# Optimization experiments

Measured on AMD Instinct MI355X. Metric: run time of the kernel, lower is better.

Reference implementation:

```python
import jax, jax.numpy as jnp
import numpy as np

T, B, A = 128, 512, 5
X, Y, Z, H, R = 2, 10, 32, 128, 128
LOG2PI = np.float32(np.log(2.0 * np.pi))


def setup_inputs() -> dict:
    key = jax.random.key(0)
    ks = iter(jax.random.split(key, 40))
    w = lambda *s: jax.random.normal(next(ks), s, jnp.float32) * 0.05
    return dict(
        states=jax.random.normal(next(ks), (T, B, Y), jnp.float32),
        eps=jax.random.normal(next(ks), (T - 1, B, A, Z), jnp.float32),
        enc_w1=w(A, X + Y + R, H), enc_b1=w(A, H),
        enc_w2=w(A, H, H), enc_b2=w(A, H),
        enc_mw=w(A, H, Z), enc_mb=w(A, Z),
        enc_sw=w(A, H, Z), enc_sb=w(A, Z),
        pri_w1=w(A, Y + R, H), pri_b1=w(A, H),
        pri_w2=w(A, H, H), pri_b2=w(A, H),
        pri_mw=w(A, H, Z), pri_mb=w(A, Z),
        pri_sw=w(A, H, Z), pri_sb=w(A, Z),
        dec_w1=w(A, Y + Z + R, H), dec_b1=w(A, H),
        dec_w2=w(A, H, H), dec_b2=w(A, H),
        dec_mw=w(A, H, X), dec_mb=w(A, X),
        dec_sw=w(A, H, X), dec_sb=w(A, X),
        gru_wih=w(A, X + Z, 3 * R), gru_whh=w(A, R, 3 * R),
        gru_bih=w(A, 3 * R), gru_bhh=w(A, 3 * R),
    )


def _lin(x, wt, b):
    # x: [B, A, I], wt: [A, I, O] -> [B, A, O]  (per-agent linear)
    return jnp.einsum('bai,aio->bao', x, wt) + b


def _mlp(x, w1, b1, w2, b2):
    return jax.nn.relu(_lin(jax.nn.relu(_lin(x, w1, b1)), w2, b2))


def reference(states, eps, enc_w1, enc_b1, enc_w2, enc_b2, enc_mw, enc_mb,
              enc_sw, enc_sb, pri_w1, pri_b1, pri_w2, pri_b2, pri_mw, pri_mb,
              pri_sw, pri_sb, dec_w1, dec_b1, dec_w2, dec_b2, dec_mw, dec_mb,
              dec_sw, dec_sb, gru_wih, gru_whh, gru_bih, gru_bhh):
    y_all = states[:-1]                              # [T-1, B, Y]
    x_all = states[1:].reshape(T - 1, B, A, X)       # per-agent next positions

    def step(carry, xs):
        h, kl, nll = carry                           # h: [B, A, R]
        y, x, e = xs                                 # y:[B,Y] x:[B,A,X] e:[B,A,Z]
        yb = jnp.broadcast_to(y[:, None, :], (B, A, Y))
        enc_h = _mlp(jnp.concatenate([x, yb, h], -1), enc_w1, enc_b1, enc_w2, enc_b2)
        enc_m = _lin(enc_h, enc_mw, enc_mb)
        enc_s = jax.nn.softplus(_lin(enc_h, enc_sw, enc_sb))
        pri_h = _mlp(jnp.concatenate([yb, h], -1), pri_w1, pri_b1, pri_w2, pri_b2)
        pri_m = _lin(pri_h, pri_mw, pri_mb)
        pri_s = jax.nn.softplus(_lin(pri_h, pri_sw, pri_sb))
        z = enc_m + enc_s * e                         # reparameterized sample
        dec_h = _mlp(jnp.concatenate([yb, z, h], -1), dec_w1, dec_b1, dec_w2, dec_b2)
        dec_m = _lin(dec_h, dec_mw, dec_mb)
        dec_s = jax.nn.softplus(_lin(dec_h, dec_sw, dec_sb))
        # GRU cell (torch gate order: r, z, n)
        gi = _lin(jnp.concatenate([x, z], -1), gru_wih, gru_bih)   # [B,A,3R]
        gh = _lin(h, gru_whh, gru_bhh)
        gir, giz, gin = jnp.split(gi, 3, -1)
        ghr, ghz, ghn = jnp.split(gh, 3, -1)
        r = jax.nn.sigmoid(gir + ghr)
        u = jax.nn.sigmoid(giz + ghz)
        n = jnp.tanh(gin + r * ghn)
        h_new = (1.0 - u) * n + u * h
        kl_t = 0.5 * jnp.sum(2.0 * jnp.log(pri_s) - 2.0 * jnp.log(enc_s)
                             + (enc_s ** 2 + (enc_m - pri_m) ** 2) / pri_s ** 2 - 1.0)
        nll_t = jnp.sum(0.5 * LOG2PI + jnp.log(dec_s) + 0.5 * ((x - dec_m) / dec_s) ** 2)
        return (h_new, kl + kl_t, nll + nll_t), None

    h0 = jnp.zeros((B, A, R), states.dtype)
    zero = jnp.zeros((), states.dtype)
    (h, kl, nll), _ = jax.lax.scan(step, (h0, zero, zero), (y_all, x_all, eps))
    return jnp.stack([kl, nll])  # [kl_loss, recon_loss]
```

## Files before the change

### kernel.cpp

```cpp
#include <hip/hip_runtime.h>

typedef __attribute__((ext_vector_type(8))) short bf16x8;
typedef __attribute__((ext_vector_type(4))) float f32x4;

#define MFMA_B16(A,B,C) __builtin_amdgcn_mfma_f32_16x16x32_bf16((A),(B),(C),0,0,0)

#define FO_ENC1 0
#define FO_PRI1 48
#define FO_DEC1 88
#define FO_GIH  136
#define FO_GHH  184
#define FO_ENC2 280
#define FO_PRI2 312
#define FO_DEC2 344
#define FO_MS   376
#define FO_DECMS 408
#define NFRAG   412

#define MS  200
#define TS  136

__device__ __forceinline__ unsigned short f2bf(float f) {
  union { float f; unsigned u; } v; v.f = f;
  unsigned r = (v.u + 0x7fffu + ((v.u >> 16) & 1u)) >> 16;
  return (unsigned short)r;
}
__device__ __forceinline__ float bf2f(unsigned short h) {
  union { unsigned u; float f; } v; v.u = ((unsigned)h) << 16;
  return v.f;
}
__device__ __forceinline__ float sigm_(float x) { return 1.f / (1.f + __expf(-x)); }
__device__ __forceinline__ float tanh_(float x) {
  x = fminf(fmaxf(x, -15.f), 15.f);
  float e = __expf(-2.f * x);
  return (1.f - e) / (1.f + e);
}
__device__ __forceinline__ float splus_(float x) {
  return fmaxf(x, 0.f) + log1pf(__expf(-fabsf(x)));
}
__device__ __forceinline__ void pin(bf16x8 &x) {
  f32x4 &r = reinterpret_cast<f32x4&>(x);
  asm volatile("" : "+v"(r));
}
__device__ __forceinline__ void pinf(float &x) { asm volatile("" : "+v"(x)); }

__global__ void prep_kernel(const float* __restrict__ ew1, const float* __restrict__ pw1,
                            const float* __restrict__ dw1, const float* __restrict__ wih,
                            const float* __restrict__ whh, const float* __restrict__ ew2,
                            const float* __restrict__ pw2, const float* __restrict__ dw2,
                            const float* __restrict__ emw, const float* __restrict__ esw,
                            const float* __restrict__ pmw, const float* __restrict__ psw,
                            const float* __restrict__ dmw, const float* __restrict__ dsw,
                            unsigned short* __restrict__ ws)
{
  int blk = blockIdx.x;
  int a = blk / NFRAG, f = blk % NFRAG;
  int l = threadIdx.x, lg = l >> 4, ln = l & 15;
  float v[8];

  if (f < FO_PRI1) {
    int fi = f, nt = fi / 6, kb = fi % 6, n = nt * 16 + ln;
#pragma unroll
    for (int j = 0; j < 8; ++j) {
      int mk = kb * 32 + lg * 8 + j;
      int r = (mk < 2) ? mk : (mk >= 34 && mk < 44) ? 2 + (mk - 34)
            : (mk >= 64) ? 12 + (mk - 64) : -1;
      v[j] = (r >= 0) ? ew1[((size_t)a * 140 + r) * 128 + n] : 0.f;
    }
  } else if (f < FO_DEC1) {
    int fi = f - FO_PRI1, nt = fi / 5, kb = 1 + fi % 5, n = nt * 16 + ln;
#pragma unroll
    for (int j = 0; j < 8; ++j) {
      int mk = kb * 32 + lg * 8 + j;
      int r = (mk >= 34 && mk < 44) ? (mk - 34) : (mk >= 64) ? 10 + (mk - 64) : -1;
      v[j] = (r >= 0) ? pw1[((size_t)a * 138 + r) * 128 + n] : 0.f;
    }
  } else if (f < FO_GIH) {
    int fi = f - FO_DEC1, nt = fi / 6, kb = fi % 6, n = nt * 16 + ln;
#pragma unroll
    for (int j = 0; j < 8; ++j) {
      int mk = kb * 32 + lg * 8 + j;
      int r = (mk >= 2 && mk < 34) ? 10 + (mk - 2) : (mk >= 34 && mk < 44) ? (mk - 34)
            : (mk >= 64) ? 42 + (mk - 64) : -1;
      v[j] = (r >= 0) ? dw1[((size_t)a * 170 + r) * 128 + n] : 0.f;
    }
  } else if (f < FO_GHH) {
    int fi = f - FO_GIH, nt = fi / 2, kb = fi % 2, n = nt * 16 + ln;
#pragma unroll
    for (int j = 0; j < 8; ++j) {
      int mk = kb * 32 + lg * 8 + j;
      v[j] = (mk < 34) ? wih[((size_t)a * 34 + mk) * 384 + n] : 0.f;
    }
  } else if (f < FO_ENC2) {
    int fi = f - FO_GHH, nt = fi / 4, kb = fi % 4, n = nt * 16 + ln;
#pragma unroll
    for (int j = 0; j < 8; ++j) {
      int r = kb * 32 + lg * 8 + j;
      v[j] = whh[((size_t)a * 128 + r) * 384 + n];
    }
  } else if (f < FO_DEC2) {
    int fi = f - FO_ENC2;
    const float* W = (fi < 32) ? ew2 : pw2;
    fi &= 31;
    int nt = fi / 4, kb = fi % 4, n = nt * 16 + ln;
#pragma unroll
    for (int j = 0; j < 8; ++j) {
      int r = kb * 32 + lg * 8 + j;
      v[j] = W[((size_t)a * 128 + r) * 128 + n];
    }
  } else if (f < FO_MS) {
    int fi = f - FO_DEC2, nt = fi / 4, kb = fi % 4, n = nt * 16 + ln;
#pragma unroll
    for (int j = 0; j < 8; ++j) {
      int r = kb * 32 + lg * 8 + j;
      v[j] = dw2[((size_t)a * 128 + r) * 128 + n];
    }
  } else if (f < FO_DECMS) {
    int fi = f - FO_MS, mat = fi / 8, rem = fi % 8, nt = rem / 4, kb = rem % 4;
    int n = nt * 16 + ln;
    const float* W = (mat == 0) ? emw : (mat == 1) ? esw : (mat == 2) ? pmw : psw;
#pragma unroll
    for (int j = 0; j < 8; ++j) {
      int r = kb * 32 + lg * 8 + j;
      v[j] = W[((size_t)a * 128 + r) * 32 + n];
    }
  } else {
    int kb = f - FO_DECMS;
#pragma unroll
    for (int j = 0; j < 8; ++j) {
      int r = kb * 32 + lg * 8 + j;
      v[j] = (ln < 2) ? dmw[((size_t)a * 128 + r) * 2 + ln]
           : (ln < 4) ? dsw[((size_t)a * 128 + r) * 2 + (ln - 2)] : 0.f;
    }
  }
  unsigned short* dst = ws + (size_t)blk * 512 + l * 8;
#pragma unroll
  for (int j = 0; j < 8; ++j) dst[j] = f2bf(v[j]);
}

__global__
__attribute__((amdgpu_flat_work_group_size(512, 512)))
__attribute__((amdgpu_waves_per_eu(2, 2)))
void vrnn_main(
    const float* __restrict__ states, const float* __restrict__ eps,
    const float* __restrict__ eb1, const float* __restrict__ eb2,
    const float* __restrict__ emb, const float* __restrict__ esb,
    const float* __restrict__ pb1, const float* __restrict__ pb2,
    const float* __restrict__ pmb, const float* __restrict__ psb,
    const float* __restrict__ db1, const float* __restrict__ db2,
    const float* __restrict__ dmb, const float* __restrict__ dsb,
    const float* __restrict__ bih, const float* __restrict__ bhh,
    const unsigned short* __restrict__ frags, float* __restrict__ out)
{
  const int a = blockIdx.y;
  const int b0 = blockIdx.x * 16;
  const int tid = threadIdx.x;
  const int w = tid >> 6, l = tid & 63, lg = l >> 4, ln = l & 15;

  __shared__ __align__(16) unsigned short ghh_lds[96 * 512];
  __shared__ __align__(16) unsigned short ms_lds[32 * 512];
  __shared__ __align__(16) unsigned short dms_lds[4 * 512];
  __shared__ __align__(16) unsigned short master[16 * MS];
  __shared__ __align__(16) unsigned short t1e[16 * TS], t1p[16 * TS];
  __shared__ __align__(16) unsigned short he[16 * TS], hp[16 * TS];
  __shared__ float msbuf[2][16][32];
  __shared__ float red[16];

  const unsigned short* fa = frags + (size_t)a * NFRAG * 512;

  {
    const uint4* s1 = (const uint4*)(fa + (size_t)FO_GHH * 512);
    uint4* d1 = (uint4*)ghh_lds;
    for (int i = tid; i < 96 * 64; i += 512) d1[i] = s1[i];
    const uint4* s2 = (const uint4*)(fa + (size_t)FO_MS * 512);
    uint4* d2 = (uint4*)ms_lds;
    for (int i = tid; i < 32 * 64; i += 512) d2[i] = s2[i];
    const uint4* s3 = (const uint4*)(fa + (size_t)FO_DECMS * 512);
    uint4* d3 = (uint4*)dms_lds;
    if (tid < 256) d3[tid] = s3[tid];
  }
  for (int i = tid; i < 16 * MS; i += 512) master[i] = 0;

  bf16x8 be1[6], bp1[5], be2[4], bp2[4], bd2[4], bD[12];
#pragma unroll
  for (int kb = 0; kb < 6; ++kb) {
    be1[kb] = *(const bf16x8*)(fa + (size_t)(FO_ENC1 + w * 6 + kb) * 512 + l * 8);
    pin(be1[kb]);
  }
#pragma unroll
  for (int kb = 0; kb < 5; ++kb) {
    bp1[kb] = *(const bf16x8*)(fa + (size_t)(FO_PRI1 + w * 5 + kb) * 512 + l * 8);
    pin(bp1[kb]);
  }
#pragma unroll
  for (int kb = 0; kb < 4; ++kb) {
    be2[kb] = *(const bf16x8*)(fa + (size_t)(FO_ENC2 + w * 4 + kb) * 512 + l * 8);
    bp2[kb] = *(const bf16x8*)(fa + (size_t)(FO_PRI2 + w * 4 + kb) * 512 + l * 8);
    bd2[kb] = *(const bf16x8*)(fa + (size_t)(FO_DEC2 + w * 4 + kb) * 512 + l * 8);
    pin(be2[kb]); pin(bp2[kb]); pin(bd2[kb]);
  }
  if (w < 4) {
#pragma unroll
    for (int j = 0; j < 2; ++j)
#pragma unroll
      for (int kb = 0; kb < 6; ++kb)
        bD[j * 6 + kb] = *(const bf16x8*)(fa + (size_t)(FO_DEC1 + (w + 4 * j) * 6 + kb) * 512 + l * 8);
  } else {
    int kx = w - 4;
#pragma unroll
    for (int g = 0; g < 3; ++g)
#pragma unroll
      for (int j = 0; j < 2; ++j)
#pragma unroll
        for (int kb = 0; kb < 2; ++kb)
          bD[g * 4 + j * 2 + kb] =
            *(const bf16x8*)(fa + (size_t)(FO_GIH + (g * 8 + kx + 4 * j) * 2 + kb) * 512 + l * 8);
  }
#pragma unroll
  for (int i = 0; i < 12; ++i) pin(bD[i]);

  float eb1v = eb1[a * 128 + w * 16 + ln], pb1v = pb1[a * 128 + w * 16 + ln];
  float eb2v = eb2[a * 128 + w * 16 + ln], pb2v = pb2[a * 128 + w * 16 + ln];
  float db2v = db2[a * 128 + w * 16 + ln];
  float hbm = 0.f, hbs = 0.f, d1b0 = 0.f, d1b1 = 0.f, dmsb = 0.f;
  float ghb[6] = {0.f, 0.f, 0.f, 0.f, 0.f, 0.f};
  if (w < 2) { hbm = emb[a * 32 + w * 16 + ln]; hbs = esb[a * 32 + w * 16 + ln]; }
  else if (w < 4) { hbm = pmb[a * 32 + (w - 2) * 16 + ln]; hbs = psb[a * 32 + (w - 2) * 16 + ln]; }
  if (w < 4) { d1b0 = db1[a * 128 + w * 16 + ln]; d1b1 = db1[a * 128 + (w + 4) * 16 + ln]; }
  else {
    int kx = w - 4;
#pragma unroll
    for (int g = 0; g < 3; ++g)
#pragma unroll
      for (int j = 0; j < 2; ++j)
        ghb[g * 2 + j] = bih[a * 384 + g * 128 + (kx + 4 * j) * 16 + ln]
                       + bhh[a * 384 + g * 128 + (kx + 4 * j) * 16 + ln];
  }
  if (w == 0) dmsb = (ln < 2) ? dmb[a * 2 + ln] : (ln < 4) ? dsb[a * 2 + (ln - 2)] : 0.f;
  pinf(eb1v); pinf(pb1v); pinf(eb2v); pinf(pb2v); pinf(db2v);
  pinf(hbm); pinf(hbs); pinf(d1b0); pinf(d1b1); pinf(dmsb);
#pragma unroll
  for (int i = 0; i < 6; ++i) pinf(ghb[i]);

  __syncthreads();

  if (tid < 160) {
    int row = tid / 10, c = tid - row * 10;
    master[row * MS + 34 + c] = f2bf(states[(size_t)b0 * 10 + tid]);
  }
  if (tid >= 192 && tid < 224) {
    int i = tid - 192, row = i >> 1, c = i & 1;
    master[row * MS + c] = f2bf(states[((size_t)512 + b0 + row) * 10 + a * 2 + c]);
  }
  float e_cur[4] = {0.f, 0.f, 0.f, 0.f};
  if (w < 2) {
#pragma unroll
    for (int q = 0; q < 4; ++q)
      e_cur[q] = eps[((size_t)(b0 + 4 * lg + q) * 5 + a) * 32 + w * 16 + ln];
  }
  float xv[4] = {0.f, 0.f, 0.f, 0.f};
  float kl = 0.f, nll = 0.f;
  f32x4 em = {0, 0, 0, 0}, esv = {0, 0, 0, 0};
  f32x4 gh[3][2];
  float hn[8];
  __syncthreads();

  for (int t = 0; t < 127; ++t) {
    if (w == 0 && t > 0) {
      f32x4 acc = {dmsb, dmsb, dmsb, dmsb};
#pragma unroll
      for (int kb = 0; kb < 4; ++kb) {
        bf16x8 ad = *(const bf16x8*)&he[ln * TS + kb * 32 + lg * 8];
        bf16x8 bf = *(const bf16x8*)&dms_lds[kb * 512 + l * 8];
        acc = MFMA_B16(ad, bf, acc);
      }
#pragma unroll
      for (int q = 0; q < 4; ++q) {
        float sv = __shfl(splus_(acc[q]), l + 2);
        if (ln < 2) {
          float d = (xv[q] - acc[q]) / sv;
          nll += 0.9189385332f + __logf(sv) + 0.5f * d * d;
        }
      }
    }
    {
      bf16x8 am[6];
#pragma unroll
      for (int kb = 0; kb < 6; ++kb)
        am[kb] = *(const bf16x8*)&master[ln * MS + kb * 32 + lg * 8];
      f32x4 a1 = {eb1v, eb1v, eb1v, eb1v}, a2 = {pb1v, pb1v, pb1v, pb1v};
#pragma unroll
      for (int kb = 0; kb < 6; ++kb) a1 = MFMA_B16(am[kb], be1[kb], a1);
#pragma unroll
      for (int kb = 0; kb < 5; ++kb) a2 = MFMA_B16(am[kb + 1], bp1[kb], a2);
#pragma unroll
      for (int q = 0; q < 4; ++q) {
        t1e[(4 * lg + q) * TS + w * 16 + ln] = f2bf(fmaxf(a1[q], 0.f));
        t1p[(4 * lg + q) * TS + w * 16 + ln] = f2bf(fmaxf(a2[q], 0.f));
      }
    }
    __syncthreads();

    {
      bf16x8 ae[4], ap[4];
#pragma unroll
      for (int kb = 0; kb < 4; ++kb) {
        ae[kb] = *(const bf16x8*)&t1e[ln * TS + kb * 32 + lg * 8];
        ap[kb] = *(const bf16x8*)&t1p[ln * TS + kb * 32 + lg * 8];
      }
      f32x4 a1 = {eb2v, eb2v, eb2v, eb2v}, a2 = {pb2v, pb2v, pb2v, pb2v};
#pragma unroll
      for (int kb = 0; kb < 4; ++kb) {
        a1 = MFMA_B16(ae[kb], be2[kb], a1);
        a2 = MFMA_B16(ap[kb], bp2[kb], a2);
      }
#pragma unroll
      for (int q = 0; q < 4; ++q) {
        he[(4 * lg + q) * TS + w * 16 + ln] = f2bf(fmaxf(a1[q], 0.f));
        hp[(4 * lg + q) * TS + w * 16 + ln] = f2bf(fmaxf(a2[q], 0.f));
      }
    }
    __syncthreads();

    {
      if (w < 4) {
        const unsigned short* hsrc = (w < 2) ? he : hp;
        bf16x8 ah[4];
#pragma unroll
        for (int kb = 0; kb < 4; ++kb)
          ah[kb] = *(const bf16x8*)&hsrc[ln * TS + kb * 32 + lg * 8];
        int mbase = ((w < 2) ? 0 : 16) + (w & 1) * 4;
        f32x4 m = {hbm, hbm, hbm, hbm}, s = {hbs, hbs, hbs, hbs};
#pragma unroll
        for (int kb = 0; kb < 4; ++kb) {
          m = MFMA_B16(ah[kb], *(const bf16x8*)&ms_lds[(mbase + kb) * 512 + l * 8], m);
          s = MFMA_B16(ah[kb], *(const bf16x8*)&ms_lds[(mbase + 8 + kb) * 512 + l * 8], s);
        }
        if (w < 2) {
          em = m;
#pragma unroll
          for (int q = 0; q < 4; ++q) {
            esv[q] = splus_(s[q]);
            master[(4 * lg + q) * MS + 2 + w * 16 + ln] = f2bf(m[q] + esv[q] * e_cur[q]);
          }
          if (t < 126) {
#pragma unroll
            for (int q = 0; q < 4; ++q)
              e_cur[q] = eps[((size_t)((t + 1) * 512 + b0 + 4 * lg + q) * 5 + a) * 32 + w * 16 + ln];
          }
        } else {
#pragma unroll
          for (int q = 0; q < 4; ++q) {
            msbuf[0][4 * lg + q][(w - 2) * 16 + ln] = m[q];
            msbuf[1][4 * lg + q][(w - 2) * 16 + ln] = splus_(s[q]);
          }
        }
      } else {
        int kx = w - 4;
        bf16x8 ahh[4];
#pragma unroll
        for (int kb = 0; kb < 4; ++kb)
          ahh[kb] = *(const bf16x8*)&master[ln * MS + (kb + 2) * 32 + lg * 8];
#pragma unroll
        for (int g = 0; g < 3; ++g)
#pragma unroll
          for (int j = 0; j < 2; ++j) {
            float bv = ghb[g * 2 + j];
            gh[g][j] = (f32x4){bv, bv, bv, bv};
          }
#pragma unroll
        for (int kb = 0; kb < 4; ++kb)
#pragma unroll
          for (int g = 0; g < 3; ++g)
#pragma unroll
            for (int j = 0; j < 2; ++j)
              gh[g][j] = MFMA_B16(ahh[kb],
                *(const bf16x8*)&ghh_lds[(size_t)((g * 8 + kx + 4 * j) * 4 + kb) * 512 + l * 8],
                gh[g][j]);
      }
    }
    __syncthreads();

    if (w == 0) {
#pragma unroll
      for (int q = 0; q < 4; ++q)
        xv[q] = states[((size_t)(t + 1) * 512 + b0 + 4 * lg + q) * 10 + a * 2 + (ln & 1)];
    }
    if (w < 4) {
      bf16x8 amn[6];
#pragma unroll
      for (int kb = 0; kb < 6; ++kb)
        amn[kb] = *(const bf16x8*)&master[ln * MS + kb * 32 + lg * 8];
#pragma unroll
      for (int j = 0; j < 2; ++j) {
        float bv = (j == 0) ? d1b0 : d1b1;
        f32x4 acc = {bv, bv, bv, bv};
#pragma unroll
        for (int kb = 0; kb < 6; ++kb) acc = MFMA_B16(amn[kb], bD[j * 6 + kb], acc);
#pragma unroll
        for (int q = 0; q < 4; ++q)
          t1e[(4 * lg + q) * TS + (w + 4 * j) * 16 + ln] = f2bf(fmaxf(acc[q], 0.f));
      }
      if (w < 2) {
#pragma unroll
        for (int q = 0; q < 4; ++q) {
          float pm = msbuf[0][4 * lg + q][w * 16 + ln];
          float ps = msbuf[1][4 * lg + q][w * 16 + ln];
          float dm = em[q] - pm;
          float es2 = esv[q] * esv[q];
          kl += 0.5f * (2.f * __logf(ps) - 2.f * __logf(esv[q]) + (es2 + dm * dm) / (ps * ps) - 1.f);
        }
      }
    } else {
      int kx = w - 4;
      bf16x8 am2[2];
#pragma unroll
      for (int kb = 0; kb < 2; ++kb)
        am2[kb] = *(const bf16x8*)&master[ln * MS + kb * 32 + lg * 8];
      f32x4 gi[3][2];
#pragma unroll
      for (int g = 0; g < 3; ++g)
#pragma unroll
        for (int j = 0; j < 2; ++j) gi[g][j] = (f32x4){0.f, 0.f, 0.f, 0.f};
#pragma unroll
      for (int kb = 0; kb < 2; ++kb)
#pragma unroll
        for (int g = 0; g < 3; ++g)
#pragma unroll
          for (int j = 0; j < 2; ++j)
            gi[g][j] = MFMA_B16(am2[kb], bD[g * 4 + j * 2 + kb], gi[g][j]);
#pragma unroll
      for (int j = 0; j < 2; ++j)
#pragma unroll
        for (int q = 0; q < 4; ++q) {
          float r_ = sigm_(gi[0][j][q] + gh[0][j][q]);
          float u_ = sigm_(gi[1][j][q] + gh[1][j][q]);
          float n_ = tanh_(gi[2][j][q] + r_ * gh[2][j][q]);
          float ho = bf2f(master[(4 * lg + q) * MS + 64 + (kx + 4 * j) * 16 + ln]);
          hn[j * 4 + q] = (1.f - u_) * n_ + u_ * ho;
        }
    }
    __syncthreads();

    {
      bf16x8 ad[4];
#pragma unroll
      for (int kb = 0; kb < 4; ++kb)
        ad[kb] = *(const bf16x8*)&t1e[ln * TS + kb * 32 + lg * 8];
      f32x4 acc = {db2v, db2v, db2v, db2v};
#pragma unroll
      for (int kb = 0; kb < 4; ++kb) acc = MFMA_B16(ad[kb], bd2[kb], acc);
#pragma unroll
      for (int q = 0; q < 4; ++q)
        he[(4 * lg + q) * TS + w * 16 + ln] = f2bf(fmaxf(acc[q], 0.f));
    }
    if (w >= 4) {
      int kx = w - 4;
#pragma unroll
      for (int j = 0; j < 2; ++j)
#pragma unroll
        for (int q = 0; q < 4; ++q)
          master[(4 * lg + q) * MS + 64 + (kx + 4 * j) * 16 + ln] = f2bf(hn[j * 4 + q]);
    }
    if (t < 126) {
      if (w >= 1 && w <= 3) {
        int i = (w - 1) * 64 + l;
        if (i < 160) {
          int row = i / 10, c = i - row * 10;
          master[row * MS + 34 + c] = f2bf(states[((size_t)(t + 1) * 512 + b0) * 10 + i]);
        }
      }
      if (w == 0 && l < 32) {
        int row = l >> 1, c = l & 1;
        master[row * MS + c] = f2bf(states[((size_t)(t + 2) * 512 + b0 + row) * 10 + a * 2 + c]);
      }
    }
    __syncthreads();
  }

  if (w == 0) {
    f32x4 acc = {dmsb, dmsb, dmsb, dmsb};
#pragma unroll
    for (int kb = 0; kb < 4; ++kb) {
      bf16x8 ad = *(const bf16x8*)&he[ln * TS + kb * 32 + lg * 8];
      bf16x8 bf = *(const bf16x8*)&dms_lds[kb * 512 + l * 8];
      acc = MFMA_B16(ad, bf, acc);
    }
#pragma unroll
    for (int q = 0; q < 4; ++q) {
      float sv = __shfl(splus_(acc[q]), l + 2);
      if (ln < 2) {
        float d = (xv[q] - acc[q]) / sv;
        nll += 0.9189385332f + __logf(sv) + 0.5f * d * d;
      }
    }
  }

#pragma unroll
  for (int off = 32; off > 0; off >>= 1) {
    kl += __shfl_down(kl, off);
    nll += __shfl_down(nll, off);
  }
  if (l == 0) { red[w] = kl; red[8 + w] = nll; }
  __syncthreads();
  if (tid == 0) {
    float K = 0.f, N = 0.f;
#pragma unroll
    for (int i = 0; i < 8; ++i) { K += red[i]; N += red[8 + i]; }
    atomicAdd(out, K);
    atomicAdd(out + 1, N);
  }
}

extern "C" void kernel_launch(void* const* d_in, const int* in_sizes, int n_in,
                              void* d_out, int out_size, void* d_ws, size_t ws_size,
                              hipStream_t stream) {
  (void)in_sizes; (void)n_in; (void)out_size; (void)ws_size;
  const float* states = (const float*)d_in[0];
  const float* eps    = (const float*)d_in[1];
  const float* ew1 = (const float*)d_in[2];
  const float* eb1 = (const float*)d_in[3];
  const float* ew2 = (const float*)d_in[4];
  const float* eb2 = (const float*)d_in[5];
  const float* emw = (const float*)d_in[6];
  const float* emb = (const float*)d_in[7];
  const float* esw = (const float*)d_in[8];
  const float* esb = (const float*)d_in[9];
  const float* pw1 = (const float*)d_in[10];
  const float* pb1 = (const float*)d_in[11];
  const float* pw2 = (const float*)d_in[12];
  const float* pb2 = (const float*)d_in[13];
  const float* pmw = (const float*)d_in[14];
  const float* pmb = (const float*)d_in[15];
  const float* psw = (const float*)d_in[16];
  const float* psb = (const float*)d_in[17];
  const float* dw1 = (const float*)d_in[18];
  const float* db1 = (const float*)d_in[19];
  const float* dw2 = (const float*)d_in[20];
  const float* db2 = (const float*)d_in[21];
  const float* dmw = (const float*)d_in[22];
  const float* dmb = (const float*)d_in[23];
  const float* dsw = (const float*)d_in[24];
  const float* dsb = (const float*)d_in[25];
  const float* wih = (const float*)d_in[26];
  const float* whh = (const float*)d_in[27];
  const float* bih = (const float*)d_in[28];
  const float* bhh = (const float*)d_in[29];

  unsigned short* frags = (unsigned short*)d_ws;
  float* out = (float*)d_out;

  hipMemsetAsync(d_out, 0, 2 * sizeof(float), stream);
  prep_kernel<<<dim3(5 * NFRAG), dim3(64), 0, stream>>>(
      ew1, pw1, dw1, wih, whh, ew2, pw2, dw2, emw, esw, pmw, psw, dmw, dsw, frags);
  vrnn_main<<<dim3(32, 5), dim3(512), 0, stream>>>(
      states, eps, eb1, eb2, emb, esb, pb1, pb2, pmb, psb,
      db1, db2, dmb, dsb, bih, bhh, frags, out);
}
```

Measured before the change: 1.183 ms.

## Halve workgroup to four waves and stream weight fragments from global each step

The main kernel drops from 8 to 4 waves per block, and each wave now computes two 16-column output tiles instead of one. The enc/pri/dec first-layer and GRU input-gate weights were pinned in registers; they are now reloaded from global memory (L2/L1) inside every timestep. The GRU gate work is merged into the same waves that do the decoder layer. This frees registers and cuts barrier participants, at the cost of repeated global fragment loads on the serial recurrence path and less parallelism per block.

Measured after the change: 1.032 ms. 1.15x faster.

```diff
diff --git a/kernel.cpp b/kernel.cpp
--- a/kernel.cpp
+++ b/kernel.cpp
@@ -17,8 +17,8 @@
 #define FO_DECMS 408
 #define NFRAG   412
 
-#define MS  200
-#define TS  136
+#define MS 200
+#define TS 136
 
 __device__ __forceinline__ unsigned short f2bf(float f) {
   union { float f; unsigned u; } v; v.f = f;
@@ -38,11 +38,6 @@
 __device__ __forceinline__ float splus_(float x) {
   return fmaxf(x, 0.f) + log1pf(__expf(-fabsf(x)));
 }
-__device__ __forceinline__ void pin(bf16x8 &x) {
-  f32x4 &r = reinterpret_cast<f32x4&>(x);
-  asm volatile("" : "+v"(r));
-}
-__device__ __forceinline__ void pinf(float &x) { asm volatile("" : "+v"(x)); }
 
 __global__ void prep_kernel(const float* __restrict__ ew1, const float* __restrict__ pw1,
                             const float* __restrict__ dw1, const float* __restrict__ wih,
@@ -138,10 +133,9 @@
   for (int j = 0; j < 8; ++j) dst[j] = f2bf(v[j]);
 }
 
-__global__
-__attribute__((amdgpu_flat_work_group_size(512, 512)))
-__attribute__((amdgpu_waves_per_eu(2, 2)))
-void vrnn_main(
+#define LD_FRAG(idx) (*(const bf16x8*)(fa + (size_t)(idx) * 512 + l * 8))
+
+__global__ __launch_bounds__(256, 1) void vrnn_main(
     const float* __restrict__ states, const float* __restrict__ eps,
     const float* __restrict__ eb1, const float* __restrict__ eb2,
     const float* __restrict__ emb, const float* __restrict__ esb,
@@ -164,83 +158,38 @@
   __shared__ __align__(16) unsigned short t1e[16 * TS], t1p[16 * TS];
   __shared__ __align__(16) unsigned short he[16 * TS], hp[16 * TS];
   __shared__ float msbuf[2][16][32];
-  __shared__ float red[16];
+  __shared__ float red[8];
 
   const unsigned short* fa = frags + (size_t)a * NFRAG * 512;
 
   {
     const uint4* s1 = (const uint4*)(fa + (size_t)FO_GHH * 512);
     uint4* d1 = (uint4*)ghh_lds;
-    for (int i = tid; i < 96 * 64; i += 512) d1[i] = s1[i];
+    for (int i = tid; i < 96 * 64; i += 256) d1[i] = s1[i];
     const uint4* s2 = (const uint4*)(fa + (size_t)FO_MS * 512);
     uint4* d2 = (uint4*)ms_lds;
-    for (int i = tid; i < 32 * 64; i += 512) d2[i] = s2[i];
+    for (int i = tid; i < 32 * 64; i += 256) d2[i] = s2[i];
     const uint4* s3 = (const uint4*)(fa + (size_t)FO_DECMS * 512);
     uint4* d3 = (uint4*)dms_lds;
-    if (tid < 256) d3[tid] = s3[tid];
-  }
-  for (int i = tid; i < 16 * MS; i += 512) master[i] = 0;
-
-  bf16x8 be1[6], bp1[5], be2[4], bp2[4], bd2[4], bD[12];
-#pragma unroll
-  for (int kb = 0; kb < 6; ++kb) {
-    be1[kb] = *(const bf16x8*)(fa + (size_t)(FO_ENC1 + w * 6 + kb) * 512 + l * 8);
-    pin(be1[kb]);
-  }
-#pragma unroll
-  for (int kb = 0; kb < 5; ++kb) {
-    bp1[kb] = *(const bf16x8*)(fa + (size_t)(FO_PRI1 + w * 5 + kb) * 512 + l * 8);
-    pin(bp1[kb]);
-  }
-#pragma unroll
-  for (int kb = 0; kb < 4; ++kb) {
-    be2[kb] = *(const bf16x8*)(fa + (size_t)(FO_ENC2 + w * 4 + kb) * 512 + l * 8);
-    bp2[kb] = *(const bf16x8*)(fa + (size_t)(FO_PRI2 + w * 4 + kb) * 512 + l * 8);
-    bd2[kb] = *(const bf16x8*)(fa + (size_t)(FO_DEC2 + w * 4 + kb) * 512 + l * 8);
-    pin(be2[kb]); pin(bp2[kb]); pin(bd2[kb]);
-  }
-  if (w < 4) {
-#pragma unroll
-    for (int j = 0; j < 2; ++j)
-#pragma unroll
-      for (int kb = 0; kb < 6; ++kb)
-        bD[j * 6 + kb] = *(const bf16x8*)(fa + (size_t)(FO_DEC1 + (w + 4 * j) * 6 + kb) * 512 + l * 8);
-  } else {
-    int kx = w - 4;
+    d3[tid] = s3[tid];
+  }
+  for (int i = tid; i < 16 * MS; i += 256) master[i] = 0;
+
+  float eb1v[2], pb1v[2], eb2v[2], pb2v[2], db2v[2], d1b[2], ghb[3][2];
+#pragma unroll
+  for (int j = 0; j < 2; ++j) {
+    int n = (w + 4 * j) * 16 + ln;
+    eb1v[j] = eb1[a * 128 + n]; pb1v[j] = pb1[a * 128 + n];
+    eb2v[j] = eb2[a * 128 + n]; pb2v[j] = pb2[a * 128 + n];
+    db2v[j] = db2[a * 128 + n]; d1b[j]  = db1[a * 128 + n];
 #pragma unroll
     for (int g = 0; g < 3; ++g)
-#pragma unroll
-      for (int j = 0; j < 2; ++j)
-#pragma unroll
-        for (int kb = 0; kb < 2; ++kb)
-          bD[g * 4 + j * 2 + kb] =
-            *(const bf16x8*)(fa + (size_t)(FO_GIH + (g * 8 + kx + 4 * j) * 2 + kb) * 512 + l * 8);
-  }
-#pragma unroll
-  for (int i = 0; i < 12; ++i) pin(bD[i]);
-
-  float eb1v = eb1[a * 128 + w * 16 + ln], pb1v = pb1[a * 128 + w * 16 + ln];
-  float eb2v = eb2[a * 128 + w * 16 + ln], pb2v = pb2[a * 128 + w * 16 + ln];
-  float db2v = db2[a * 128 + w * 16 + ln];
-  float hbm = 0.f, hbs = 0.f, d1b0 = 0.f, d1b1 = 0.f, dmsb = 0.f;
-  float ghb[6] = {0.f, 0.f, 0.f, 0.f, 0.f, 0.f};
+      ghb[g][j] = bih[a * 384 + g * 128 + n] + bhh[a * 384 + g * 128 + n];
+  }
+  float hbm, hbs, dmsb = 0.f;
   if (w < 2) { hbm = emb[a * 32 + w * 16 + ln]; hbs = esb[a * 32 + w * 16 + ln]; }
-  else if (w < 4) { hbm = pmb[a * 32 + (w - 2) * 16 + ln]; hbs = psb[a * 32 + (w - 2) * 16 + ln]; }
-  if (w < 4) { d1b0 = db1[a * 128 + w * 16 + ln]; d1b1 = db1[a * 128 + (w + 4) * 16 + ln]; }
-  else {
-    int kx = w - 4;
-#pragma unroll
-    for (int g = 0; g < 3; ++g)
-#pragma unroll
-      for (int j = 0; j < 2; ++j)
-        ghb[g * 2 + j] = bih[a * 384 + g * 128 + (kx + 4 * j) * 16 + ln]
-                       + bhh[a * 384 + g * 128 + (kx + 4 * j) * 16 + ln];
-  }
+  else { hbm = pmb[a * 32 + (w - 2) * 16 + ln]; hbs = psb[a * 32 + (w - 2) * 16 + ln]; }
   if (w == 0) dmsb = (ln < 2) ? dmb[a * 2 + ln] : (ln < 4) ? dsb[a * 2 + (ln - 2)] : 0.f;
-  pinf(eb1v); pinf(pb1v); pinf(eb2v); pinf(pb2v); pinf(db2v);
-  pinf(hbm); pinf(hbs); pinf(d1b0); pinf(d1b1); pinf(dmsb);
-#pragma unroll
-  for (int i = 0; i < 6; ++i) pinf(ghb[i]);
 
   __syncthreads();
 
@@ -284,123 +233,177 @@
       }
     }
     {
+      bf16x8 f1[12], f2[10];
+#pragma unroll
+      for (int j = 0; j < 2; ++j) {
+#pragma unroll
+        for (int kb = 0; kb < 6; ++kb) f1[j * 6 + kb] = LD_FRAG(FO_ENC1 + (w + 4 * j) * 6 + kb);
+#pragma unroll
+        for (int kb = 0; kb < 5; ++kb) f2[j * 5 + kb] = LD_FRAG(FO_PRI1 + (w + 4 * j) * 5 + kb);
+      }
       bf16x8 am[6];
 #pragma unroll
       for (int kb = 0; kb < 6; ++kb)
         am[kb] = *(const bf16x8*)&master[ln * MS + kb * 32 + lg * 8];
-      f32x4 a1 = {eb1v, eb1v, eb1v, eb1v}, a2 = {pb1v, pb1v, pb1v, pb1v};
-#pragma unroll
-      for (int kb = 0; kb < 6; ++kb) a1 = MFMA_B16(am[kb], be1[kb], a1);
-#pragma unroll
-      for (int kb = 0; kb < 5; ++kb) a2 = MFMA_B16(am[kb + 1], bp1[kb], a2);
-#pragma unroll
-      for (int q = 0; q < 4; ++q) {
-        t1e[(4 * lg + q) * TS + w * 16 + ln] = f2bf(fmaxf(a1[q], 0.f));
-        t1p[(4 * lg + q) * TS + w * 16 + ln] = f2bf(fmaxf(a2[q], 0.f));
+#pragma unroll
+      for (int j = 0; j < 2; ++j) {
+        f32x4 a1 = {eb1v[j], eb1v[j], eb1v[j], eb1v[j]};
+        f32x4 a2 = {pb1v[j], pb1v[j], pb1v[j], pb1v[j]};
+#pragma unroll
+        for (int kb = 0; kb < 6; ++kb) a1 = MFMA_B16(am[kb], f1[j * 6 + kb], a1);
+#pragma unroll
+        for (int kb = 0; kb < 5; ++kb) a2 = MFMA_B16(am[kb + 1], f2[j * 5 + kb], a2);
+#pragma unroll
+        for (int q = 0; q < 4; ++q) {
+          t1e[(4 * lg + q) * TS + (w + 4 * j) * 16 + ln] = f2bf(fmaxf(a1[q], 0.f));
+          t1p[(4 * lg + q) * TS + (w + 4 * j) * 16 + ln] = f2bf(fmaxf(a2[q], 0.f));
+        }
       }
     }
     __syncthreads();
 
     {
+      bf16x8 g1[8], g2[8];
+#pragma unroll
+      for (int j = 0; j < 2; ++j)
+#pragma unroll
+        for (int kb = 0; kb < 4; ++kb) {
+          g1[j * 4 + kb] = LD_FRAG(FO_ENC2 + (w + 4 * j) * 4 + kb);
+          g2[j * 4 + kb] = LD_FRAG(FO_PRI2 + (w + 4 * j) * 4 + kb);
+        }
       bf16x8 ae[4], ap[4];
 #pragma unroll
       for (int kb = 0; kb < 4; ++kb) {
         ae[kb] = *(const bf16x8*)&t1e[ln * TS + kb * 32 + lg * 8];
         ap[kb] = *(const bf16x8*)&t1p[ln * TS + kb * 32 + lg * 8];
       }
-      f32x4 a1 = {eb2v, eb2v, eb2v, eb2v}, a2 = {pb2v, pb2v, pb2v, pb2v};
+#pragma unroll
+      for (int j = 0; j < 2; ++j) {
+        f32x4 a1 = {eb2v[j], eb2v[j], eb2v[j], eb2v[j]};
+        f32x4 a2 = {pb2v[j], pb2v[j], pb2v[j], pb2v[j]};
+#pragma unroll
+        for (int kb = 0; kb < 4; ++kb) {
+          a1 = MFMA_B16(ae[kb], g1[j * 4 + kb], a1);
+          a2 = MFMA_B16(ap[kb], g2[j * 4 + kb], a2);
+        }
+#pragma unroll
+        for (int q = 0; q < 4; ++q) {
+          he[(4 * lg + q) * TS + (w + 4 * j) * 16 + ln] = f2bf(fmaxf(a1[q], 0.f));
+          hp[(4 * lg + q) * TS + (w + 4 * j) * 16 + ln] = f2bf(fmaxf(a2[q], 0.f));
+        }
+      }
+    }
+    __syncthreads();
+
+    {
+      const unsigned short* hs = (w < 2) ? he : hp;
+      int mbase = ((w < 2) ? 0 : 16) + (w & 1) * 4;
+      bf16x8 ah[4];
+#pragma unroll
+      for (int kb = 0; kb < 4; ++kb)
+        ah[kb] = *(const bf16x8*)&hs[ln * TS + kb * 32 + lg * 8];
+      f32x4 m = {hbm, hbm, hbm, hbm}, s = {hbs, hbs, hbs, hbs};
 #pragma unroll
       for (int kb = 0; kb < 4; ++kb) {
-        a1 = MFMA_B16(ae[kb], be2[kb], a1);
-        a2 = MFMA_B16(ap[kb], bp2[kb], a2);
-      }
-#pragma unroll
-      for (int q = 0; q < 4; ++q) {
-        he[(4 * lg + q) * TS + w * 16 + ln] = f2bf(fmaxf(a1[q], 0.f));
-        hp[(4 * lg + q) * TS + w * 16 + ln] = f2bf(fmaxf(a2[q], 0.f));
-      }
+        m = MFMA_B16(ah[kb], *(const bf16x8*)&ms_lds[(mbase + kb) * 512 + l * 8], m);
+        s = MFMA_B16(ah[kb], *(const bf16x8*)&ms_lds[(mbase + 8 + kb) * 512 + l * 8], s);
+      }
+      if (w < 2) {
+        em = m;
+#pragma unroll
+        for (int q = 0; q < 4; ++q) {
+          esv[q] = splus_(s[q]);
+          master[(4 * lg + q) * MS + 2 + w * 16 + ln] = f2bf(m[q] + esv[q] * e_cur[q]);
+        }
+        if (t < 126) {
+#pragma unroll
+          for (int q = 0; q < 4; ++q)
+            e_cur[q] = eps[((size_t)((t + 1) * 512 + b0 + 4 * lg + q) * 5 + a) * 32 + w * 16 + ln];
+        }
+      } else {
+#pragma unroll
+        for (int q = 0; q < 4; ++q) {
+          msbuf[0][4 * lg + q][(w - 2) * 16 + ln] = m[q];
+          msbuf[1][4 * lg + q][(w - 2) * 16 + ln] = splus_(s[q]);
+        }
+      }
+      bf16x8 ahh[4];
+#pragma unroll
+      for (int kb = 0; kb < 4; ++kb)
+        ahh[kb] = *(const bf16x8*)&master[ln * MS + (kb + 2) * 32 + lg * 8];
+#pragma unroll
+      for (int g = 0; g < 3; ++g)
+#pragma unroll
+        for (int j = 0; j < 2; ++j) {
+          float bv = ghb[g][j];
+          gh[g][j] = (f32x4){bv, bv, bv, bv};
+        }
+#pragma unroll
+      for (int kb = 0; kb < 4; ++kb)
+#pragma unroll
+        for (int g = 0; g < 3; ++g)
+#pragma unroll
+          for (int j = 0; j < 2; ++j)
+            gh[g][j] = MFMA_B16(ahh[kb],
+              *(const bf16x8*)&ghh_lds[(size_t)((g * 8 + w + 4 * j) * 4 + kb) * 512 + l * 8],
+              gh[g][j]);
     }
     __syncthreads();
 
     {
-      if (w < 4) {
-        const unsigned short* hsrc = (w < 2) ? he : hp;
-        bf16x8 ah[4];
-#pragma unroll
-        for (int kb = 0; kb < 4; ++kb)
-          ah[kb] = *(const bf16x8*)&hsrc[ln * TS + kb * 32 + lg * 8];
-        int mbase = ((w < 2) ? 0 : 16) + (w & 1) * 4;
-        f32x4 m = {hbm, hbm, hbm, hbm}, s = {hbs, hbs, hbs, hbs};
-#pragma unroll
-        for (int kb = 0; kb < 4; ++kb) {
-          m = MFMA_B16(ah[kb], *(const bf16x8*)&ms_lds[(mbase + kb) * 512 + l * 8], m);
-          s = MFMA_B16(ah[kb], *(const bf16x8*)&ms_lds[(mbase + 8 + kb) * 512 + l * 8], s);
-        }
-        if (w < 2) {
-          em = m;
-#pragma unroll
-          for (int q = 0; q < 4; ++q) {
-            esv[q] = splus_(s[q]);
-            master[(4 * lg + q) * MS + 2 + w * 16 + ln] = f2bf(m[q] + esv[q] * e_cur[q]);
-          }
-          if (t < 126) {
-#pragma unroll
-            for (int q = 0; q < 4; ++q)
-              e_cur[q] = eps[((size_t)((t + 1) * 512 + b0 + 4 * lg + q) * 5 + a) * 32 + w * 16 + ln];
-          }
-        } else {
-#pragma unroll
-          for (int q = 0; q < 4; ++q) {
-            msbuf[0][4 * lg + q][(w - 2) * 16 + ln] = m[q];
-            msbuf[1][4 * lg + q][(w - 2) * 16 + ln] = splus_(s[q]);
-          }
-        }
-      } else {
-        int kx = w - 4;
-        bf16x8 ahh[4];
-#pragma unroll
-        for (int kb = 0; kb < 4; ++kb)
-          ahh[kb] = *(const bf16x8*)&master[ln * MS + (kb + 2) * 32 + lg * 8];
-#pragma unroll
-        for (int g = 0; g < 3; ++g)
-#pragma unroll
-          for (int j = 0; j < 2; ++j) {
-            float bv = ghb[g * 2 + j];
-            gh[g][j] = (f32x4){bv, bv, bv, bv};
-          }
-#pragma unroll
-        for (int kb = 0; kb < 4; ++kb)
-#pragma unroll
-          for (int g = 0; g < 3; ++g)
-#pragma unroll
-            for (int j = 0; j < 2; ++j)
-              gh[g][j] = MFMA_B16(ahh[kb],
-                *(const bf16x8*)&ghh_lds[(size_t)((g * 8 + kx + 4 * j) * 4 + kb) * 512 + l * 8],
-                gh[g][j]);
-      }
-    }
-    __syncthreads();
-
-    if (w == 0) {
-#pragma unroll
-      for (int q = 0; q < 4; ++q)
-        xv[q] = states[((size_t)(t + 1) * 512 + b0 + 4 * lg + q) * 10 + a * 2 + (ln & 1)];
-    }
-    if (w < 4) {
-      bf16x8 amn[6];
+      if (w == 0) {
+#pragma unroll
+        for (int q = 0; q < 4; ++q)
+          xv[q] = states[((size_t)(t + 1) * 512 + b0 + 4 * lg + q) * 10 + a * 2 + (ln & 1)];
+      }
+      bf16x8 fd[12], fg[12];
+#pragma unroll
+      for (int j = 0; j < 2; ++j)
+#pragma unroll
+        for (int kb = 0; kb < 6; ++kb)
+          fd[j * 6 + kb] = LD_FRAG(FO_DEC1 + (w + 4 * j) * 6 + kb);
+#pragma unroll
+      for (int g = 0; g < 3; ++g)
+#pragma unroll
+        for (int j = 0; j < 2; ++j)
+#pragma unroll
+          for (int kb = 0; kb < 2; ++kb)
+            fg[g * 4 + j * 2 + kb] = LD_FRAG(FO_GIH + (g * 8 + w + 4 * j) * 2 + kb);
+      bf16x8 am[6];
 #pragma unroll
       for (int kb = 0; kb < 6; ++kb)
-        amn[kb] = *(const bf16x8*)&master[ln * MS + kb * 32 + lg * 8];
+        am[kb] = *(const bf16x8*)&master[ln * MS + kb * 32 + lg * 8];
 #pragma unroll
       for (int j = 0; j < 2; ++j) {
-        float bv = (j == 0) ? d1b0 : d1b1;
-        f32x4 acc = {bv, bv, bv, bv};
-#pragma unroll
-        for (int kb = 0; kb < 6; ++kb) acc = MFMA_B16(amn[kb], bD[j * 6 + kb], acc);
+        f32x4 acc = {d1b[j], d1b[j], d1b[j], d1b[j]};
+#pragma unroll
+        for (int kb = 0; kb < 6; ++kb) acc = MFMA_B16(am[kb], fd[j * 6 + kb], acc);
 #pragma unroll
         for (int q = 0; q < 4; ++q)
           t1e[(4 * lg + q) * TS + (w + 4 * j) * 16 + ln] = f2bf(fmaxf(acc[q], 0.f));
       }
+      f32x4 gi[3][2];
+#pragma unroll
+      for (int g = 0; g < 3; ++g)
+#pragma unroll
+        for (int j = 0; j < 2; ++j) gi[g][j] = (f32x4){0.f, 0.f, 0.f, 0.f};
+#pragma unroll
+      for (int kb = 0; kb < 2; ++kb)
+#pragma unroll
+        for (int g = 0; g < 3; ++g)
+#pragma unroll
+          for (int j = 0; j < 2; ++j)
+            gi[g][j] = MFMA_B16(am[kb], fg[g * 4 + j * 2 + kb], gi[g][j]);
+#pragma unroll
+      for (int j = 0; j < 2; ++j)
+#pragma unroll
+        for (int q = 0; q < 4; ++q) {
+          float r_ = sigm_(gi[0][j][q] + gh[0][j][q]);
+          float u_ = sigm_(gi[1][j][q] + gh[1][j][q]);
+          float n_ = tanh_(gi[2][j][q] + r_ * gh[2][j][q]);
+          float ho = bf2f(master[(4 * lg + q) * MS + 64 + (w + 4 * j) * 16 + ln]);
+          hn[j * 4 + q] = (1.f - u_) * n_ + u_ * ho;
+        }
       if (w < 2) {
 #pragma unroll
         for (int q = 0; q < 4; ++q) {
@@ -411,68 +414,46 @@
           kl += 0.5f * (2.f * __logf(ps) - 2.f * __logf(esv[q]) + (es2 + dm * dm) / (ps * ps) - 1.f);
         }
       }
-    } else {
-      int kx = w - 4;
-      bf16x8 am2[2];
-#pragma unroll
-      for (int kb = 0; kb < 2; ++kb)
-        am2[kb] = *(const bf16x8*)&master[ln * MS + kb * 32 + lg * 8];
-      f32x4 gi[3][2];
-#pragma unroll
-      for (int g = 0; g < 3; ++g)
-#pragma unroll
-        for (int j = 0; j < 2; ++j) gi[g][j] = (f32x4){0.f, 0.f, 0.f, 0.f};
-#pragma unroll
-      for (int kb = 0; kb < 2; ++kb)
-#pragma unroll
-        for (int g = 0; g < 3; ++g)
-#pragma unroll
-          for (int j = 0; j < 2; ++j)
-            gi[g][j] = MFMA_B16(am2[kb], bD[g * 4 + j * 2 + kb], gi[g][j]);
+    }
+    __syncthreads();
+
+    {
+      bf16x8 fd2[8];
 #pragma unroll
       for (int j = 0; j < 2; ++j)
 #pragma unroll
-        for (int q = 0; q < 4; ++q) {
-          float r_ = sigm_(gi[0][j][q] + gh[0][j][q]);
-          float u_ = sigm_(gi[1][j][q] + gh[1][j][q]);
-          float n_ = tanh_(gi[2][j][q] + r_ * gh[2][j][q]);
-          float ho = bf2f(master[(4 * lg + q) * MS + 64 + (kx + 4 * j) * 16 + ln]);
-          hn[j * 4 + q] = (1.f - u_) * n_ + u_ * ho;
-        }
-    }
-    __syncthreads();
-
-    {
+        for (int kb = 0; kb < 4; ++kb)
+          fd2[j * 4 + kb] = LD_FRAG(FO_DEC2 + (w + 4 * j) * 4 + kb);
       bf16x8 ad[4];
 #pragma unroll
       for (int kb = 0; kb < 4; ++kb)
         ad[kb] = *(const bf16x8*)&t1e[ln * TS + kb * 32 + lg * 8];
-      f32x4 acc = {db2v, db2v, db2v, db2v};
-#pragma unroll
-      for (int kb = 0; kb < 4; ++kb) acc = MFMA_B16(ad[kb], bd2[kb], acc);
-#pragma unroll
-      for (int q = 0; q < 4; ++q)
-        he[(4 * lg + q) * TS + w * 16 + ln] = f2bf(fmaxf(acc[q], 0.f));
-    }
-    if (w >= 4) {
-      int kx = w - 4;
+#pragma unroll
+      for (int j = 0; j < 2; ++j) {
+        f32x4 acc = {db2v[j], db2v[j], db2v[j], db2v[j]};
+#pragma unroll
+        for (int kb = 0; kb < 4; ++kb) acc = MFMA_B16(ad[kb], fd2[j * 4 + kb], acc);
+#pragma unroll
+        for (int q = 0; q < 4; ++q)
+          he[(4 * lg + q) * TS + (w + 4 * j) * 16 + ln] = f2bf(fmaxf(acc[q], 0.f));
+      }
 #pragma unroll
       for (int j = 0; j < 2; ++j)
 #pragma unroll
         for (int q = 0; q < 4; ++q)
-          master[(4 * lg + q) * MS + 64 + (kx + 4 * j) * 16 + ln] = f2bf(hn[j * 4 + q]);
-    }
-    if (t < 126) {
-      if (w >= 1 && w <= 3) {
-        int i = (w - 1) * 64 + l;
-        if (i < 160) {
-          int row = i / 10, c = i - row * 10;
-          master[row * MS + 34 + c] = f2bf(states[((size_t)(t + 1) * 512 + b0) * 10 + i]);
-        }
-      }
-      if (w == 0 && l < 32) {
-        int row = l >> 1, c = l & 1;
-        master[row * MS + c] = f2bf(states[((size_t)(t + 2) * 512 + b0 + row) * 10 + a * 2 + c]);
+          master[(4 * lg + q) * MS + 64 + (w + 4 * j) * 16 + ln] = f2bf(hn[j * 4 + q]);
+      if (t < 126) {
+        if (w >= 1) {
+          int i = (w - 1) * 64 + l;
+          if (i < 160) {
+            int row = i / 10, c = i - row * 10;
+            master[row * MS + 34 + c] = f2bf(states[((size_t)(t + 1) * 512 + b0) * 10 + i]);
+          }
+        }
+        if (w == 0 && l < 32) {
+          int row = l >> 1, c = l & 1;
+          master[row * MS + c] = f2bf(states[((size_t)(t + 2) * 512 + b0 + row) * 10 + a * 2 + c]);
+        }
       }
     }
     __syncthreads();
@@ -501,12 +482,12 @@
     kl += __shfl_down(kl, off);
     nll += __shfl_down(nll, off);
   }
-  if (l == 0) { red[w] = kl; red[8 + w] = nll; }
+  if (l == 0) { red[w] = kl; red[4 + w] = nll; }
   __syncthreads();
   if (tid == 0) {
     float K = 0.f, N = 0.f;
 #pragma unroll
-    for (int i = 0; i < 8; ++i) { K += red[i]; N += red[8 + i]; }
+    for (int i = 0; i < 4; ++i) { K += red[i]; N += red[4 + i]; }
     atomicAdd(out, K);
     atomicAdd(out + 1, N);
   }
@@ -553,7 +534,7 @@
   hipMemsetAsync(d_out, 0, 2 * sizeof(float), stream);
   prep_kernel<<<dim3(5 * NFRAG), dim3(64), 0, stream>>>(
       ew1, pw1, dw1, wih, whh, ew2, pw2, dw2, emw, esw, pmw, psw, dmw, dsw, frags);
-  vrnn_main<<<dim3(32, 5), dim3(512), 0, stream>>>(
+  vrnn_main<<<dim3(32, 5), dim3(256), 0, stream>>>(
       states, eps, eb1, eb2, emb, esb, pb1, pb2, pmb, psb,
       db1, db2, dmb, dsb, bih, bhh, frags, out);
 }
```
